# Kernel optimization log

Measured on AMD Instinct MI355X. Metric: run time of the kernel, lower is better.

## Reference

```python
import jax, jax.numpy as jnp
import numpy as np

V = 50000  # vocab size
S = 200    # tokens per phrase
B = 2048   # number of phrases


def setup_inputs() -> dict:
    key = jax.random.key(0)
    k1, k2, k3 = jax.random.split(key, 3)
    text = jax.random.randint(k1, (S, B), 0, V, dtype=jnp.int64)
    w_weight = jax.random.normal(k2, (1, V), dtype=jnp.float32)
    w_bias = jax.random.normal(k3, (1,), dtype=jnp.float32)
    return {"text": text, "w_weight": w_weight, "w_bias": w_bias}


def reference(text, w_weight, w_bias):
    # word_vecs[phrase, val] += count(val in phrase)  (counts=True path)
    S_, B_ = text.shape
    phrase_idx = jnp.broadcast_to(jnp.arange(B_)[None, :], (S_, B_))
    word_vecs = jnp.zeros((B_, w_weight.shape[1]), dtype=w_weight.dtype)
    word_vecs = word_vecs.at[phrase_idx, text].add(1.0)
    # tiny linear layer: [B, V] @ [V, 1] + bias
    return word_vecs @ w_weight.T + w_bias
```

## Files before the change

### kernel.cpp

```cpp
#include <hip/hip_runtime.h>
#include <hip/hip_bf16.h>


#define VV 50000
#define SS 200
#define BB 2048
#define CHUNK 8

__global__ __launch_bounds__(256) void MNB_455266533601_kernel(
    const int* __restrict__ text,
    const float* __restrict__ w,
    const float* __restrict__ bias,
    float* __restrict__ out)
{
    const int b  = blockIdx.x * 256 + threadIdx.x;
    const int s0 = blockIdx.y * CHUNK;

    float sum = 0.0f;
#pragma unroll
    for (int k = 0; k < CHUNK; ++k) {
        const int idx = text[(s0 + k) * BB + b];
        sum += w[idx];
    }
    if (blockIdx.y == 0) sum += bias[0];
    atomicAdd(&out[b], sum);
}

extern "C" void kernel_launch(void* const* d_in, const int* in_sizes, int n_in,
                              void* d_out, int out_size, void* d_ws, size_t ws_size,
                              hipStream_t stream) {
    const int*   text = (const int*)  d_in[0];
    const float* w    = (const float*)d_in[1];
    const float* bias = (const float*)d_in[2];
    float* out = (float*)d_out;

    hipMemsetAsync(out, 0, (size_t)out_size * sizeof(float), stream);

    dim3 grid(BB / 256, SS / CHUNK, 1);
    dim3 block(256, 1, 1);
    MNB_455266533601_kernel<<<grid, block, 0, stream>>>(text, w, bias, out);
}
```

Baseline: 60.36 us.

## Replace atomic split-S accumulation with per-block shared-memory reduction, drop memset

Each block now handles 8 phrases across all 200 tokens. The 32 thread groups each sum a contiguous slice of about 6-7 tokens and reduce the partial sums in shared memory, so the output is written once without atomics. This removes the separate memset launch and the global atomicAdd traffic. In exchange, each warp reads the text array with only 8 contiguous ints (32 bytes) per row, which worsens coalescing, and the grid grows to 256 small blocks.

After: 59.72 us. About the same (-1.1%).

```diff
diff --git a/kernel.cpp b/kernel.cpp
--- a/kernel.cpp
+++ b/kernel.cpp
@@ -1,11 +1,12 @@
 #include <hip/hip_runtime.h>
-#include <hip/hip_bf16.h>
 
 
 #define VV 50000
 #define SS 200
 #define BB 2048
-#define CHUNK 8
+#define NB 8
+#define NCHUNK 32
+#define MAXC 7
 
 __global__ __launch_bounds__(256) void MNB_455266533601_kernel(
     const int* __restrict__ text,
@@ -13,17 +14,32 @@
     const float* __restrict__ bias,
     float* __restrict__ out)
 {
-    const int b  = blockIdx.x * 256 + threadIdx.x;
-    const int s0 = blockIdx.y * CHUNK;
+    const int tid = threadIdx.x;
+    const int bl  = tid & (NB - 1);
+    const int c   = tid >> 3;
+    const int b   = blockIdx.x * NB + bl;
+    const int s0  = (c * SS) >> 5;
+    const int s1  = ((c + 1) * SS) >> 5;
 
     float sum = 0.0f;
 #pragma unroll
-    for (int k = 0; k < CHUNK; ++k) {
-        const int idx = text[(s0 + k) * BB + b];
-        sum += w[idx];
+    for (int k = 0; k < MAXC; ++k) {
+        const int s = s0 + k;
+        if (s < s1)
+            sum += w[text[s * BB + b]];
     }
-    if (blockIdx.y == 0) sum += bias[0];
-    atomicAdd(&out[b], sum);
+
+    __shared__ float part[NCHUNK][NB];
+    part[c][bl] = sum;
+    __syncthreads();
+
+    if (tid < NB) {
+        float t = bias[0];
+#pragma unroll
+        for (int cc = 0; cc < NCHUNK; ++cc)
+            t += part[cc][bl];
+        out[b] = t;
+    }
 }
 
 extern "C" void kernel_launch(void* const* d_in, const int* in_sizes, int n_in,
@@ -34,9 +50,7 @@
     const float* bias = (const float*)d_in[2];
     float* out = (float*)d_out;
 
-    hipMemsetAsync(out, 0, (size_t)out_size * sizeof(float), stream);
-
-    dim3 grid(BB / 256, SS / CHUNK, 1);
-    dim3 block(256, 1, 1);
+    dim3 grid(BB / NB, 1, 1);
+    dim3 block(NB * NCHUNK, 1, 1);
     MNB_455266533601_kernel<<<grid, block, 0, stream>>>(text, w, bias, out);
 }
```
